# Optimization experiments

Hardware: AMD Instinct MI355X
Metric: run time of the kernel (lower is better)

## Reference

```python
import jax, jax.numpy as jnp
import numpy as np

BETA = 0.9       # snn.Leaky(beta=0.9)
THRESH = 1.0     # snntorch default threshold, reset_mechanism='subtract'


def setup_inputs() -> dict:
    key = jax.random.key(0)
    ks = jax.random.split(key, 7)
    B = 16384
    return {
        "x":  jax.random.normal(ks[0], (B, 1700), dtype=jnp.float32),
        "W1": jax.random.normal(ks[1], (64, 1700), dtype=jnp.float32) * 0.02,
        "b1": jax.random.normal(ks[2], (64,), dtype=jnp.float32) * 0.02,
        "W2": jax.random.normal(ks[3], (32, 64), dtype=jnp.float32) * 0.1,
        "b2": jax.random.normal(ks[4], (32,), dtype=jnp.float32) * 0.1,
        "W3": jax.random.normal(ks[5], (2, 32), dtype=jnp.float32) * 0.1,
        "b3": jax.random.normal(ks[6], (2,), dtype=jnp.float32) * 0.1,
        "num_steps": 20,
    }


def _lif_step(mem, cur):
    # snntorch Leaky: reset (subtract) based on previous mem crossing threshold,
    # then leaky integration of the new input current.
    reset = (mem > THRESH).astype(mem.dtype)
    return BETA * mem + cur - reset * THRESH


def reference(x, W1, b1, W2, b2, W3, b3, num_steps):
    B = x.shape[0]
    # Dropout is identity in eval mode; x is constant across steps, so cur1 is
    # loop-invariant and computed once (same math as the original loop).
    cur1 = x @ W1.T + b1                         # [B, 64]

    def step(carry, _):
        mem1, mem2 = carry
        mem1 = _lif_step(mem1, cur1)             # [B, 64]
        cur2 = mem1 @ W2.T + b2                  # [B, 32]
        mem2 = _lif_step(mem2, cur2)             # [B, 32]
        return (mem1, mem2), None

    init = (jnp.zeros((B, 64), x.dtype), jnp.zeros((B, 32), x.dtype))
    (mem1, mem2), _ = jax.lax.scan(step, init, None, length=num_steps)
    return mem2 @ W3.T + b3                      # [B, 2]
```

## Files before the change

kernel.cpp:

```cpp
#include <hip/hip_runtime.h>
#include <hip/hip_bf16.h>

typedef float f32x4 __attribute__((ext_vector_type(4)));
typedef short bf16x8 __attribute__((ext_vector_type(8)));

#define MFMA16 __builtin_amdgcn_mfma_f32_16x16x32_bf16

static constexpr int KDIM = 1700;
static constexpr int NKT2 = 56;
static constexpr float BETA = 0.9f;
static constexpr float THRESH = 1.0f;

__device__ __forceinline__ void split_bf(float f, short& hi, short& lo) {
    __hip_bfloat16 h = __float2bfloat16(f);
    float r = f - __bfloat162float(h);
    __hip_bfloat16 l = __float2bfloat16(r);
    hi = (short)__builtin_bit_cast(unsigned short, h);
    lo = (short)__builtin_bit_cast(unsigned short, l);
}

__device__ __forceinline__ void split8(f32x4 a, f32x4 b, bf16x8& hi, bf16x8& lo) {
    #pragma unroll
    for (int i = 0; i < 4; ++i) { short h, l; split_bf(a[i], h, l); hi[i] = h; lo[i] = l; }
    #pragma unroll
    for (int i = 0; i < 4; ++i) { short h, l; split_bf(b[i], h, l); hi[4 + i] = h; lo[4 + i] = l; }
}

__global__ void w1_relayout(const float* __restrict__ W1,
                            short* __restrict__ WTh, short* __restrict__ WTl) {
    const int g    = blockIdx.x * 256 + threadIdx.x;
    const int kt   = g >> 8;
    const int nt   = (g >> 6) & 3;
    const int lane = g & 63;
    const int n    = nt * 16 + (lane & 15);
    const int kb   = kt * 32 + (lane >> 4) * 8;
    bf16x8 vh, vl;
    #pragma unroll
    for (int i = 0; i < 8; ++i) {
        const int k = kb + i;
        const float v = (k < KDIM) ? W1[n * KDIM + k] : 0.f;
        short h, l; split_bf(v, h, l);
        vh[i] = h; vl[i] = l;
    }
    *(bf16x8*)(WTh + (size_t)g * 8) = vh;
    *(bf16x8*)(WTl + (size_t)g * 8) = vl;
}

__device__ __forceinline__ void gll16(const short* src, const short* lds_dst) {
    __builtin_amdgcn_global_load_lds(
        (const __attribute__((address_space(1))) unsigned int*)src,
        (__attribute__((address_space(3))) unsigned int*)lds_dst, 16, 0, 0);
}

__global__ __launch_bounds__(256, 2) void snn_fused(
    const float* __restrict__ x,
    const short* __restrict__ WTh, const short* __restrict__ WTl,
    const float* __restrict__ b1, const float* __restrict__ W2,
    const float* __restrict__ b2, const float* __restrict__ W3,
    const float* __restrict__ b3, const int* __restrict__ nsp,
    float* __restrict__ out)
{
    __shared__ __align__(16) char smemraw[65536];
    short* ldsW = (short*)smemraw;
    float (*red)[32][68] = (float (*)[32][68])smemraw;

    const int tid = threadIdx.x;
    const int wid = tid >> 6;
    const int lane = tid & 63;
    const int l15 = lane & 15;
    const int g4  = lane >> 4;
    const int kg  = g4 * 8;
    const int rowBase = blockIdx.x * 32;
    const int t0  = wid * 14;

    const float* xr0 = x + (size_t)(rowBase + l15) * KDIM;
    const float* xr1 = xr0 + (size_t)16 * KDIM;
    const short* pWh = WTh + (size_t)t0 * 2048 + lane * 8;
    const short* pWl = WTl + (size_t)t0 * 2048 + lane * 8;
    short* myLds = ldsW + wid * 8192;

    struct XB { f32x4 a0, a1, b0, b1; };
    auto xload = [&](int t, XB& xb) {
        const int k1 = t * 32 + kg;
        const int kc1 = (k1 <= 1696) ? k1 : 1664;
        const int kc2 = (k1 + 4 <= 1696) ? k1 + 4 : 1664;
        const float* p0 = xr0 + kc1;
        const float* p1 = xr0 + kc2;
        const float* p2 = xr1 + kc1;
        const float* p3 = xr1 + kc2;
        asm volatile("global_load_dwordx4 %0, %1, off" : "=v"(xb.a0) : "v"(p0));
        asm volatile("global_load_dwordx4 %0, %1, off" : "=v"(xb.a1) : "v"(p1));
        asm volatile("global_load_dwordx4 %0, %1, off" : "=v"(xb.b0) : "v"(p2));
        asm volatile("global_load_dwordx4 %0, %1, off" : "=v"(xb.b1) : "v"(p3));
    };
    auto stageW = [&](int i, int buf) {
        short* dstb = myLds + buf * 4096;
        #pragma unroll
        for (int q = 0; q < 4; ++q) {
            gll16(pWh + (size_t)i * 2048 + q * 512, dstb + q * 512);
            gll16(pWl + (size_t)i * 2048 + q * 512, dstb + 2048 + q * 512);
        }
    };

    f32x4 acc[2][4] = {};
    XB x0, x1, x2;

    stageW(0, 0);
    xload(t0 + 0, x0);
    xload(t0 + 1, x1);
    stageW(1, 1);
    xload(t0 + 2, x2);

#define GSTEP(I, XC, WAITN)                                                    \
    {                                                                          \
        asm volatile("s_waitcnt vmcnt(" #WAITN ")" ::: "memory");              \
        __builtin_amdgcn_sched_barrier(0);                                     \
        const short* rb = myLds + ((I) & 1) * 4096;                            \
        bf16x8 WC[8];                                                          \
        _Pragma("unroll")                                                      \
        for (int q = 0; q < 8; ++q)                                            \
            WC[q] = *(const bf16x8*)(rb + q * 512 + lane * 8);                 \
        bf16x8 ah0, al0, ah1, al1;                                             \
        split8(XC.a0, XC.a1, ah0, al0);                                        \
        split8(XC.b0, XC.b1, ah1, al1);                                        \
        asm volatile("s_waitcnt lgkmcnt(0)" ::: "memory");                     \
        __builtin_amdgcn_sched_barrier(0);                                     \
        if constexpr ((I) + 2 < 14) stageW((I) + 2, (I) & 1);                  \
        if constexpr ((I) + 3 < 14) xload(t0 + (I) + 3, XC);                   \
        __builtin_amdgcn_sched_barrier(0);                                     \
        _Pragma("unroll")                                                      \
        for (int nt = 0; nt < 4; ++nt) {                                       \
            acc[0][nt] = MFMA16(ah0, WC[nt],     acc[0][nt], 0, 0, 0);         \
            acc[0][nt] = MFMA16(al0, WC[nt],     acc[0][nt], 0, 0, 0);         \
            acc[0][nt] = MFMA16(ah0, WC[4 + nt], acc[0][nt], 0, 0, 0);         \
            acc[1][nt] = MFMA16(ah1, WC[nt],     acc[1][nt], 0, 0, 0);         \
            acc[1][nt] = MFMA16(al1, WC[nt],     acc[1][nt], 0, 0, 0);         \
            acc[1][nt] = MFMA16(ah1, WC[4 + nt], acc[1][nt], 0, 0, 0);         \
        }                                                                      \
    }

    GSTEP(0,  x0, 16)
    GSTEP(1,  x1, 16)
    GSTEP(2,  x2, 16)
    GSTEP(3,  x0, 16)
    GSTEP(4,  x1, 16)
    GSTEP(5,  x2, 16)
    GSTEP(6,  x0, 16)
    GSTEP(7,  x1, 16)
    GSTEP(8,  x2, 16)
    GSTEP(9,  x0, 16)
    GSTEP(10, x1, 16)
    GSTEP(11, x2, 16)
    GSTEP(12, x0, 12)
    GSTEP(13, x1, 0)
#undef GSTEP

    __syncthreads();

    #pragma unroll
    for (int mt = 0; mt < 2; ++mt)
        #pragma unroll
        for (int nt = 0; nt < 4; ++nt)
            #pragma unroll
            for (int j = 0; j < 4; ++j)
                red[wid][mt * 16 + g4 * 4 + j][nt * 16 + l15] = acc[mt][nt][j];
    __syncthreads();

    {
        const int rr  = tid >> 3;
        const int seg = tid & 7;
        f32x4 s0 = *(const f32x4*)(b1 + seg * 8);
        f32x4 s1 = *(const f32x4*)(b1 + seg * 8 + 4);
        #pragma unroll
        for (int p = 0; p < 4; ++p) {
            s0 += *(const f32x4*)&red[p][rr][seg * 8];
            s1 += *(const f32x4*)&red[p][rr][seg * 8 + 4];
        }
        *(f32x4*)&red[0][rr][seg * 8]     = s0;
        *(f32x4*)&red[0][rr][seg * 8 + 4] = s1;
    }
    __syncthreads();
    if (wid >= 2) return;

    const int lrow = wid * 16 + l15;

    float c1[2][8], c1m1[2][8];
    #pragma unroll
    for (int kt = 0; kt < 2; ++kt) {
        f32x4 u0 = *(const f32x4*)&red[0][lrow][kt * 32 + kg];
        f32x4 u1 = *(const f32x4*)&red[0][lrow][kt * 32 + kg + 4];
        #pragma unroll
        for (int i = 0; i < 4; ++i) {
            c1[kt][i] = u0[i];     c1[kt][4 + i] = u1[i];
            c1m1[kt][i] = u0[i] - THRESH; c1m1[kt][4 + i] = u1[i] - THRESH;
        }
    }

    bf16x8 W2hf[2][2], W2lf[2][2];
    #pragma unroll
    for (int rt = 0; rt < 2; ++rt)
        #pragma unroll
        for (int kt = 0; kt < 2; ++kt) {
            const float* wp = W2 + (rt * 16 + l15) * 64 + kt * 32 + kg;
            split8(*(const f32x4*)wp, *(const f32x4*)(wp + 4), W2hf[rt][kt], W2lf[rt][kt]);
        }

    float b2v[2][4], b2m1[2][4], w3a[2][4], w3b[2][4];
    #pragma unroll
    for (int nt = 0; nt < 2; ++nt)
        #pragma unroll
        for (int j = 0; j < 4; ++j) {
            const int o = nt * 16 + g4 * 4 + j;
            b2v[nt][j]  = b2[o];
            b2m1[nt][j] = b2[o] - THRESH;
            w3a[nt][j] = W3[o];
            w3b[nt][j] = W3[32 + o];
        }

    float m1[2][8] = {};
    float m2[2][4] = {};
    const int ns = nsp[0];
    for (int s = 0; s < ns; ++s) {
        bf16x8 mh[2], ml[2];
        #pragma unroll
        for (int kt = 0; kt < 2; ++kt)
            #pragma unroll
            for (int i = 0; i < 8; ++i) {
                float m = m1[kt][i];
                m = __builtin_fmaf(BETA, m, (m > THRESH) ? c1m1[kt][i] : c1[kt][i]);
                m1[kt][i] = m;
                short h, l; split_bf(m, h, l);
                mh[kt][i] = h; ml[kt][i] = l;
            }
        f32x4 a2[2][2] = {};
        #pragma unroll
        for (int rt = 0; rt < 2; ++rt)
            #pragma unroll
            for (int kt = 0; kt < 2; ++kt) {
                a2[rt][kt] = MFMA16(W2hf[rt][kt], mh[kt], a2[rt][kt], 0, 0, 0);
                a2[rt][kt] = MFMA16(W2lf[rt][kt], mh[kt], a2[rt][kt], 0, 0, 0);
                a2[rt][kt] = MFMA16(W2hf[rt][kt], ml[kt], a2[rt][kt], 0, 0, 0);
            }
        #pragma unroll
        for (int nt = 0; nt < 2; ++nt) {
            f32x4 c2 = a2[nt][0] + a2[nt][1];
            #pragma unroll
            for (int j = 0; j < 4; ++j) {
                float m = m2[nt][j];
                m2[nt][j] = __builtin_fmaf(
                    BETA, m, c2[j] + ((m > THRESH) ? b2m1[nt][j] : b2v[nt][j]));
            }
        }
    }

    float p0 = 0.f, p1 = 0.f;
    #pragma unroll
    for (int nt = 0; nt < 2; ++nt)
        #pragma unroll
        for (int j = 0; j < 4; ++j) {
            p0 = __builtin_fmaf(m2[nt][j], w3a[nt][j], p0);
            p1 = __builtin_fmaf(m2[nt][j], w3b[nt][j], p1);
        }
    p0 += __shfl_xor(p0, 16); p0 += __shfl_xor(p0, 32);
    p1 += __shfl_xor(p1, 16); p1 += __shfl_xor(p1, 32);
    if (lane < 16) {
        const size_t row = rowBase + lrow;
        out[row * 2 + 0] = p0 + b3[0];
        out[row * 2 + 1] = p1 + b3[1];
    }
}

extern "C" void kernel_launch(void* const* d_in, const int* in_sizes, int n_in,
                              void* d_out, int out_size, void* d_ws, size_t ws_size,
                              hipStream_t stream) {
    const float* x  = (const float*)d_in[0];
    const float* W1 = (const float*)d_in[1];
    const float* b1 = (const float*)d_in[2];
    const float* W2 = (const float*)d_in[3];
    const float* b2 = (const float*)d_in[4];
    const float* W3 = (const float*)d_in[5];
    const float* b3 = (const float*)d_in[6];
    const int*   ns = (const int*)d_in[7];
    float* o = (float*)d_out;

    const int B = in_sizes[0] / KDIM;
    short* WTh  = (short*)d_ws;
    short* WTl  = WTh + (size_t)NKT2 * 2048;

    w1_relayout<<<NKT2, 256, 0, stream>>>(W1, WTh, WTl);
    snn_fused<<<B / 32, 256, 0, stream>>>(x, WTh, WTl, b1, W2, b2, W3, b3, ns, o);
}
```

Measured before the change: 43.93 us.

## Split fused kernel into split-K GEMM and separate recurrence kernel

The fused kernel is split in two. The first is a split-K GEMM in which each 512-thread block loads its whole 7-tile K slice of W1 into LDS once and reuses it across 8 waves of rows, writing partial sums for 8 K-slices to workspace. The second kernel sums those partials with the bias and runs the LIF recurrence using all its waves. This removes the per-wave W1 streaming and the LDS reduction from the old kernel, at the cost of an extra launch and 32 MB of partial-sum writes and reads through global memory.

```diff
diff --git a/kernel.cpp b/kernel.cpp
--- a/kernel.cpp
+++ b/kernel.cpp
@@ -52,36 +52,41 @@
         (__attribute__((address_space(3))) unsigned int*)lds_dst, 16, 0, 0);
 }
 
-__global__ __launch_bounds__(256, 2) void snn_fused(
+__global__ __launch_bounds__(512, 1) void gemmq(
     const float* __restrict__ x,
     const short* __restrict__ WTh, const short* __restrict__ WTl,
-    const float* __restrict__ b1, const float* __restrict__ W2,
-    const float* __restrict__ b2, const float* __restrict__ W3,
-    const float* __restrict__ b3, const int* __restrict__ nsp,
-    float* __restrict__ out)
+    float* __restrict__ pcur)
 {
-    __shared__ __align__(16) char smemraw[65536];
-    short* ldsW = (short*)smemraw;
-    float (*red)[32][68] = (float (*)[32][68])smemraw;
-
-    const int tid = threadIdx.x;
-    const int wid = tid >> 6;
+    __shared__ __align__(16) short ldsW[7 * 4096];
+    const int tid  = threadIdx.x;
+    const int wid  = tid >> 6;
     const int lane = tid & 63;
-    const int l15 = lane & 15;
-    const int g4  = lane >> 4;
-    const int kg  = g4 * 8;
-    const int rowBase = blockIdx.x * 32;
-    const int t0  = wid * 14;
+    const int l15  = lane & 15;
+    const int g4   = lane >> 4;
+    const int kg   = g4 * 8;
+    const int e    = blockIdx.x & 7;
+    const int rgrp = blockIdx.x >> 3;
+    const int rowBase = rgrp * 256 + wid * 32;
+    const int tb   = e * 7;
+
+    #pragma unroll
+    for (int c = 0; c < 7; ++c) {
+        const int chunk = wid * 7 + c;
+        const int tile  = chunk >> 3;
+        const int q     = chunk & 7;
+        const short* src = (q < 4)
+            ? WTh + (size_t)(tb + tile) * 2048 + q * 512
+            : WTl + (size_t)(tb + tile) * 2048 + (q - 4) * 512;
+        short* dst = ldsW + tile * 4096 + ((q < 4) ? q * 512 : 2048 + (q - 4) * 512);
+        gll16(src + lane * 8, dst);
+    }
 
     const float* xr0 = x + (size_t)(rowBase + l15) * KDIM;
     const float* xr1 = xr0 + (size_t)16 * KDIM;
-    const short* pWh = WTh + (size_t)t0 * 2048 + lane * 8;
-    const short* pWl = WTl + (size_t)t0 * 2048 + lane * 8;
-    short* myLds = ldsW + wid * 8192;
 
     struct XB { f32x4 a0, a1, b0, b1; };
     auto xload = [&](int t, XB& xb) {
-        const int k1 = t * 32 + kg;
+        const int k1  = t * 32 + kg;
         const int kc1 = (k1 <= 1696) ? k1 : 1664;
         const int kc2 = (k1 + 4 <= 1696) ? k1 + 4 : 1664;
         const float* p0 = xr0 + kc1;
@@ -93,29 +98,23 @@
         asm volatile("global_load_dwordx4 %0, %1, off" : "=v"(xb.b0) : "v"(p2));
         asm volatile("global_load_dwordx4 %0, %1, off" : "=v"(xb.b1) : "v"(p3));
     };
-    auto stageW = [&](int i, int buf) {
-        short* dstb = myLds + buf * 4096;
-        #pragma unroll
-        for (int q = 0; q < 4; ++q) {
-            gll16(pWh + (size_t)i * 2048 + q * 512, dstb + q * 512);
-            gll16(pWl + (size_t)i * 2048 + q * 512, dstb + 2048 + q * 512);
-        }
-    };
+
+    XB x0, x1, x2;
+    xload(tb + 0, x0);
+    xload(tb + 1, x1);
+    xload(tb + 2, x2);
+
+    asm volatile("s_waitcnt vmcnt(12)" ::: "memory");
+    __builtin_amdgcn_sched_barrier(0);
+    __builtin_amdgcn_s_barrier();
 
     f32x4 acc[2][4] = {};
-    XB x0, x1, x2;
-
-    stageW(0, 0);
-    xload(t0 + 0, x0);
-    xload(t0 + 1, x1);
-    stageW(1, 1);
-    xload(t0 + 2, x2);
-
-#define GSTEP(I, XC, WAITN)                                                    \
+
+#define QSTEP(I, XC, WAITN)                                                    \
     {                                                                          \
         asm volatile("s_waitcnt vmcnt(" #WAITN ")" ::: "memory");              \
         __builtin_amdgcn_sched_barrier(0);                                     \
-        const short* rb = myLds + ((I) & 1) * 4096;                            \
+        const short* rb = ldsW + (I) * 4096;                                   \
         bf16x8 WC[8];                                                          \
         _Pragma("unroll")                                                      \
         for (int q = 0; q < 8; ++q)                                            \
@@ -123,10 +122,8 @@
         bf16x8 ah0, al0, ah1, al1;                                             \
         split8(XC.a0, XC.a1, ah0, al0);                                        \
         split8(XC.b0, XC.b1, ah1, al1);                                        \
+        if constexpr ((I) + 3 < 7) xload(tb + (I) + 3, XC);                    \
         asm volatile("s_waitcnt lgkmcnt(0)" ::: "memory");                     \
-        __builtin_amdgcn_sched_barrier(0);                                     \
-        if constexpr ((I) + 2 < 14) stageW((I) + 2, (I) & 1);                  \
-        if constexpr ((I) + 3 < 14) xload(t0 + (I) + 3, XC);                   \
         __builtin_amdgcn_sched_barrier(0);                                     \
         _Pragma("unroll")                                                      \
         for (int nt = 0; nt < 4; ++nt) {                                       \
@@ -139,60 +136,54 @@
         }                                                                      \
     }
 
-    GSTEP(0,  x0, 16)
-    GSTEP(1,  x1, 16)
-    GSTEP(2,  x2, 16)
-    GSTEP(3,  x0, 16)
-    GSTEP(4,  x1, 16)
-    GSTEP(5,  x2, 16)
-    GSTEP(6,  x0, 16)
-    GSTEP(7,  x1, 16)
-    GSTEP(8,  x2, 16)
-    GSTEP(9,  x0, 16)
-    GSTEP(10, x1, 16)
-    GSTEP(11, x2, 16)
-    GSTEP(12, x0, 12)
-    GSTEP(13, x1, 0)
-#undef GSTEP
-
-    __syncthreads();
-
+    QSTEP(0, x0, 8)
+    QSTEP(1, x1, 8)
+    QSTEP(2, x2, 8)
+    QSTEP(3, x0, 8)
+    QSTEP(4, x1, 8)
+    QSTEP(5, x2, 4)
+    QSTEP(6, x0, 0)
+#undef QSTEP
+
+    float* pq = pcur + ((size_t)e << 20) + (size_t)rowBase * 64;
     #pragma unroll
     for (int mt = 0; mt < 2; ++mt)
         #pragma unroll
         for (int nt = 0; nt < 4; ++nt)
             #pragma unroll
             for (int j = 0; j < 4; ++j)
-                red[wid][mt * 16 + g4 * 4 + j][nt * 16 + l15] = acc[mt][nt][j];
-    __syncthreads();
-
-    {
-        const int rr  = tid >> 3;
-        const int seg = tid & 7;
-        f32x4 s0 = *(const f32x4*)(b1 + seg * 8);
-        f32x4 s1 = *(const f32x4*)(b1 + seg * 8 + 4);
-        #pragma unroll
-        for (int p = 0; p < 4; ++p) {
-            s0 += *(const f32x4*)&red[p][rr][seg * 8];
-            s1 += *(const f32x4*)&red[p][rr][seg * 8 + 4];
-        }
-        *(f32x4*)&red[0][rr][seg * 8]     = s0;
-        *(f32x4*)&red[0][rr][seg * 8 + 4] = s1;
-    }
-    __syncthreads();
-    if (wid >= 2) return;
-
-    const int lrow = wid * 16 + l15;
+                pq[(mt * 16 + g4 * 4 + j) * 64 + nt * 16 + l15] = acc[mt][nt][j];
+}
+
+__global__ __launch_bounds__(256, 2) void recur(
+    const float* __restrict__ pcur, const float* __restrict__ b1,
+    const float* __restrict__ W2, const float* __restrict__ b2,
+    const float* __restrict__ W3, const float* __restrict__ b3,
+    const int* __restrict__ nsp, float* __restrict__ out)
+{
+    const int tid = threadIdx.x;
+    const int wid = tid >> 6;
+    const int lane = tid & 63;
+    const int l15 = lane & 15;
+    const int g4  = lane >> 4;
+    const int kg  = g4 * 8;
+    const int row = blockIdx.x * 64 + wid * 16 + l15;
 
     float c1[2][8], c1m1[2][8];
     #pragma unroll
     for (int kt = 0; kt < 2; ++kt) {
-        f32x4 u0 = *(const f32x4*)&red[0][lrow][kt * 32 + kg];
-        f32x4 u1 = *(const f32x4*)&red[0][lrow][kt * 32 + kg + 4];
+        f32x4 s0 = *(const f32x4*)(b1 + kt * 32 + kg);
+        f32x4 s1 = *(const f32x4*)(b1 + kt * 32 + kg + 4);
+        #pragma unroll
+        for (int e = 0; e < 8; ++e) {
+            const float* pp = pcur + ((size_t)e << 20) + (size_t)row * 64 + kt * 32 + kg;
+            s0 += *(const f32x4*)pp;
+            s1 += *(const f32x4*)(pp + 4);
+        }
         #pragma unroll
         for (int i = 0; i < 4; ++i) {
-            c1[kt][i] = u0[i];     c1[kt][4 + i] = u1[i];
-            c1m1[kt][i] = u0[i] - THRESH; c1m1[kt][4 + i] = u1[i] - THRESH;
+            c1[kt][i] = s0[i];            c1[kt][4 + i] = s1[i];
+            c1m1[kt][i] = s0[i] - THRESH; c1m1[kt][4 + i] = s1[i] - THRESH;
         }
     }
 
@@ -264,9 +255,8 @@
     p0 += __shfl_xor(p0, 16); p0 += __shfl_xor(p0, 32);
     p1 += __shfl_xor(p1, 16); p1 += __shfl_xor(p1, 32);
     if (lane < 16) {
-        const size_t row = rowBase + lrow;
-        out[row * 2 + 0] = p0 + b3[0];
-        out[row * 2 + 1] = p1 + b3[1];
+        out[(size_t)row * 2 + 0] = p0 + b3[0];
+        out[(size_t)row * 2 + 1] = p1 + b3[1];
     }
 }
 
@@ -286,7 +276,9 @@
     const int B = in_sizes[0] / KDIM;
     short* WTh  = (short*)d_ws;
     short* WTl  = WTh + (size_t)NKT2 * 2048;
+    float* pcur = (float*)((char*)d_ws + (2 << 20));
 
     w1_relayout<<<NKT2, 256, 0, stream>>>(W1, WTh, WTl);
-    snn_fused<<<B / 32, 256, 0, stream>>>(x, WTh, WTl, b1, W2, b2, W3, b3, ns, o);
-}
+    gemmq<<<8 * (B / 256), 512, 0, stream>>>(x, WTh, WTl, pcur);
+    recur<<<B / 64, 256, 0, stream>>>(pcur, b1, W2, b2, W3, b3, ns, o);
+}
```

Measured after the change: 50.18 us. +14.2%, slower.

## Coalesce x loads by row and transpose through swizzled LDS

Applied to the files above, without the earlier changes.

x is now fetched so that eight consecutive lanes read one contiguous 128-byte row segment, instead of each lane reading scattered 16-byte pieces across sixteen rows. The tile is written to a per-wave LDS region with an XOR swizzle and read back in the MFMA operand layout before the bf16 hi/lo split. The aim is better global-memory coalescing on this bandwidth-bound first GEMM. In exchange it adds an LDS write/read round trip and extra lgkmcnt waits each step, and grows LDS to 80 KB per block, which may limit occupancy.

```diff
diff --git a/kernel.cpp b/kernel.cpp
--- a/kernel.cpp
+++ b/kernel.cpp
@@ -60,9 +60,10 @@
     const float* __restrict__ b3, const int* __restrict__ nsp,
     float* __restrict__ out)
 {
-    __shared__ __align__(16) char smemraw[65536];
-    short* ldsW = (short*)smemraw;
-    float (*red)[32][68] = (float (*)[32][68])smemraw;
+    __shared__ __align__(16) char smem[81920];
+    short* ldsW = (short*)smem;
+    char*  ldsX = smem + 65536;
+    float (*red)[32][68] = (float (*)[32][68])smem;
 
     const int tid = threadIdx.x;
     const int wid = tid >> 6;
@@ -73,28 +74,29 @@
     const int rowBase = blockIdx.x * 32;
     const int t0  = wid * 14;
 
-    const float* xr0 = x + (size_t)(rowBase + l15) * KDIM;
-    const float* xr1 = xr0 + (size_t)16 * KDIM;
     const short* pWh = WTh + (size_t)t0 * 2048 + lane * 8;
     const short* pWl = WTl + (size_t)t0 * 2048 + lane * 8;
-    short* myLds = ldsW + wid * 8192;
-
-    struct XB { f32x4 a0, a1, b0, b1; };
+    short* myLdsW = ldsW + wid * 8192;
+    char*  myLdsX = ldsX + wid * 4096;
+
+    const char* xbase = (const char*)(x + (size_t)(rowBase + (lane >> 3)) * KDIM)
+                        + (lane & 7) * 16;
+    char* xwr = myLdsX + (lane >> 3) * 128 + (((lane & 7) ^ (lane >> 3)) << 4);
+
+    struct XB { f32x4 v0, v1, v2, v3; };
     auto xload = [&](int t, XB& xb) {
-        const int k1 = t * 32 + kg;
-        const int kc1 = (k1 <= 1696) ? k1 : 1664;
-        const int kc2 = (k1 + 4 <= 1696) ? k1 + 4 : 1664;
-        const float* p0 = xr0 + kc1;
-        const float* p1 = xr0 + kc2;
-        const float* p2 = xr1 + kc1;
-        const float* p3 = xr1 + kc2;
-        asm volatile("global_load_dwordx4 %0, %1, off" : "=v"(xb.a0) : "v"(p0));
-        asm volatile("global_load_dwordx4 %0, %1, off" : "=v"(xb.a1) : "v"(p1));
-        asm volatile("global_load_dwordx4 %0, %1, off" : "=v"(xb.b0) : "v"(p2));
-        asm volatile("global_load_dwordx4 %0, %1, off" : "=v"(xb.b1) : "v"(p3));
+        const int cb = (t < 53 || (t == 53 && (lane & 7) == 0)) ? t * 128 : 52 * 128;
+        const char* p0 = xbase + cb;
+        const char* p1 = p0 + (size_t)8 * KDIM * 4;
+        const char* p2 = p0 + (size_t)16 * KDIM * 4;
+        const char* p3 = p0 + (size_t)24 * KDIM * 4;
+        asm volatile("global_load_dwordx4 %0, %1, off" : "=v"(xb.v0) : "v"(p0));
+        asm volatile("global_load_dwordx4 %0, %1, off" : "=v"(xb.v1) : "v"(p1));
+        asm volatile("global_load_dwordx4 %0, %1, off" : "=v"(xb.v2) : "v"(p2));
+        asm volatile("global_load_dwordx4 %0, %1, off" : "=v"(xb.v3) : "v"(p3));
     };
     auto stageW = [&](int i, int buf) {
-        short* dstb = myLds + buf * 4096;
+        short* dstb = myLdsW + buf * 4096;
         #pragma unroll
         for (int q = 0; q < 4; ++q) {
             gll16(pWh + (size_t)i * 2048 + q * 512, dstb + q * 512);
@@ -111,23 +113,37 @@
     stageW(1, 1);
     xload(t0 + 2, x2);
 
+    const int sw0 = ((2 * g4)     ^ (l15 & 7)) << 4;
+    const int sw1 = ((2 * g4 + 1) ^ (l15 & 7)) << 4;
+    char* xrd = myLdsX + l15 * 128;
+
 #define GSTEP(I, XC, WAITN)                                                    \
     {                                                                          \
         asm volatile("s_waitcnt vmcnt(" #WAITN ")" ::: "memory");              \
         __builtin_amdgcn_sched_barrier(0);                                     \
-        const short* rb = myLds + ((I) & 1) * 4096;                            \
+        *(f32x4*)(xwr)          = XC.v0;                                       \
+        *(f32x4*)(xwr + 1024)   = XC.v1;                                       \
+        *(f32x4*)(xwr + 2048)   = XC.v2;                                       \
+        *(f32x4*)(xwr + 3072)   = XC.v3;                                       \
+        const short* rb = myLdsW + ((I) & 1) * 4096;                           \
         bf16x8 WC[8];                                                          \
         _Pragma("unroll")                                                      \
         for (int q = 0; q < 8; ++q)                                            \
             WC[q] = *(const bf16x8*)(rb + q * 512 + lane * 8);                 \
-        bf16x8 ah0, al0, ah1, al1;                                             \
-        split8(XC.a0, XC.a1, ah0, al0);                                        \
-        split8(XC.b0, XC.b1, ah1, al1);                                        \
+        asm volatile("s_waitcnt lgkmcnt(0)" ::: "memory");                     \
+        __builtin_amdgcn_sched_barrier(0);                                     \
+        f32x4 a0 = *(const f32x4*)(xrd + sw0);                                 \
+        f32x4 a1 = *(const f32x4*)(xrd + sw1);                                 \
+        f32x4 b0 = *(const f32x4*)(xrd + 2048 + sw0);                          \
+        f32x4 b1 = *(const f32x4*)(xrd + 2048 + sw1);                          \
         asm volatile("s_waitcnt lgkmcnt(0)" ::: "memory");                     \
         __builtin_amdgcn_sched_barrier(0);                                     \
         if constexpr ((I) + 2 < 14) stageW((I) + 2, (I) & 1);                  \
         if constexpr ((I) + 3 < 14) xload(t0 + (I) + 3, XC);                   \
         __builtin_amdgcn_sched_barrier(0);                                     \
+        bf16x8 ah0, al0, ah1, al1;                                             \
+        split8(a0, a1, ah0, al0);                                              \
+        split8(b0, b1, ah1, al1);                                              \
         _Pragma("unroll")                                                      \
         for (int nt = 0; nt < 4; ++nt) {                                       \
             acc[0][nt] = MFMA16(ah0, WC[nt],     acc[0][nt], 0, 0, 0);         \
```

Result: slower. 44.91 us (+2.2%).
